# Kernel tuning notes

Hardware: AMD Instinct MI355X
Metric: run time of the kernel (lower is better)

The kernel has to match this reference:

```python
import jax, jax.numpy as jnp
import numpy as np

E, D, H, K = 8, 2048, 1024, 2  # num_experts, input_size, hidden_size, top_k
B, L = 2, 1024


def setup_inputs() -> dict:
    key = jax.random.key(0)
    k1, k2, k3, k4 = jax.random.split(key, 4)
    x = jax.random.normal(k1, (B, L, D), dtype=jnp.float32)
    w_gate = jax.random.normal(k2, (E, D), dtype=jnp.float32) * 0.02   # router Linear weight [E, D]
    w_in = jax.random.normal(k3, (E, 2 * H, D), dtype=jnp.float32) * 0.02  # ParallelExperts [E, out=2H, in=D]
    w_out = jax.random.normal(k4, (E, D, H), dtype=jnp.float32) * 0.02     # ParallelExperts [E, out=D, in=H]
    bias = jnp.zeros((D,), dtype=jnp.float32)
    return {"x": x, "w_gate": w_gate, "w_in": w_in, "w_out": w_out, "bias": bias}


def _moe_forward(x, w_gate, w_in, w_out, bias):
    bsz, length, d = x.shape
    xt = x.reshape(-1, d)  # [T, D]
    # top-k router: logits -> top-k -> softmax over selected logits
    logits = xt @ w_gate.T  # [T, E]
    topk_vals, topk_idx = jax.lax.top_k(logits, K)  # [T, K]
    topk_gates = jax.nn.softmax(topk_vals, axis=-1)  # [T, K]
    T = xt.shape[0]
    # dense [T, E] gate matrix; zero for non-selected experts, so the dense
    # per-expert compute below is mathematically identical to gathered dispatch
    gates = jnp.zeros((T, E), dtype=xt.dtype).at[jnp.arange(T)[:, None], topk_idx].add(topk_gates)
    # expert GLU FFN, vectorized over experts
    h = jnp.einsum('td,efd->tef', xt, w_in)  # [T, E, 2H]
    h1, h2 = jnp.split(h, 2, axis=-1)
    a = jax.nn.silu(h1) * h2                 # [T, E, H]
    eo = jnp.einsum('teh,edh->ted', a, w_out)  # [T, E, D]
    y = jnp.einsum('ted,te->td', eo, gates) + bias
    return y.reshape(bsz, length, d)


def reference(x, w_gate, w_in, w_out, bias):
    y = _moe_forward(x, w_gate, w_in, w_out, bias)
    loss = jnp.float32(0.0)  # router aux loss is 0 in eval mode (JetMoE top_k_gating)
    return (y, loss)
```

## Files before the change

kernel.cpp:

```cpp
#include <hip/hip_runtime.h>
#include <hip/hip_bf16.h>

#define E_    8
#define D_    2048
#define H_    1024
#define T_    2048
#define BK    64

using u16   = unsigned short;
using s16x8 = __attribute__((ext_vector_type(8))) short;
using f32x4 = __attribute__((ext_vector_type(4))) float;

#define WAITVM0 asm volatile("s_waitcnt vmcnt(0)" ::: "memory")

__device__ __forceinline__ short f2bf(float f) {
  __hip_bfloat16 h = __float2bfloat16(f);
  return __builtin_bit_cast(short, h);
}
__device__ __forceinline__ int slot(int r, int c) { return r * 64 + ((c ^ (r & 7)) << 3); }

__device__ __forceinline__ void gload16(const void* g, void* l) {
  __builtin_amdgcn_global_load_lds((const __attribute__((address_space(1))) void*)g,
                                   (__attribute__((address_space(3))) void*)l, 16, 0, 0);
}

#define FIND_EXPERT(ml, cnt, e, mt, Ne)                        \
  { int b_ = 0;                                                \
    _Pragma("unroll")                                          \
    for (int i_ = 0; i_ < E_; ++i_) {                          \
      int ti_ = (cnt[i_] + 127) >> 7;                          \
      if ((ml) >= b_ && (ml) < b_ + ti_) {                     \
        e = i_; mt = (ml) - b_; Ne = cnt[i_]; }                \
      b_ += ti_; } }


#define WIN_ELEMS  33554432
#define WTOT_ELEMS 50331648

__global__ __launch_bounds__(256) void prep_kernel(
    const float* __restrict__ x, const float* __restrict__ wg,
    const float* __restrict__ w_in, const float* __restrict__ w_out,
    const float* __restrict__ bias,
    u16* __restrict__ xb, u16* __restrict__ wb_in, u16* __restrict__ wb_out,
    int* __restrict__ lists, float* __restrict__ gates, int* __restrict__ counts,
    float* __restrict__ out)
{
  int t = blockIdx.x;
  int tid = threadIdx.x;

#pragma unroll
  for (int j = 0; j < 12; ++j) {
    int idx = t * 24576 + j * 2048 + tid * 8;
    const float* src; u16* dst;
    if (idx < WIN_ELEMS) { src = w_in + idx;  dst = wb_in + idx; }
    else                 { src = w_out + (idx - WIN_ELEMS); dst = wb_out + (idx - WIN_ELEMS); }
    f32x4 a = *(const f32x4*)(src);
    f32x4 b = *(const f32x4*)(src + 4);
    s16x8 o;
    o[0]=f2bf(a.x); o[1]=f2bf(a.y); o[2]=f2bf(a.z); o[3]=f2bf(a.w);
    o[4]=f2bf(b.x); o[5]=f2bf(b.y); o[6]=f2bf(b.z); o[7]=f2bf(b.w);
    *(s16x8*)dst = o;
  }

  {
    const float* bp = bias + tid * 8;
    f32x4 b0 = *(const f32x4*)(bp), b1 = *(const f32x4*)(bp + 4);
    *(f32x4*)(out + (size_t)t * D_ + tid * 8)     = b0;
    *(f32x4*)(out + (size_t)t * D_ + tid * 8 + 4) = b1;
    if (t == 0 && tid == 0) out[(size_t)T_ * D_] = 0.0f;
  }

  const float* xr = x + (size_t)t * D_;
  float acc[E_];
#pragma unroll
  for (int e = 0; e < E_; ++e) acc[e] = 0.f;
#pragma unroll
  for (int i = 0; i < D_ / 256; ++i) {
    int d = tid + 256 * i;
    float xv = xr[d];
    xb[(size_t)t * D_ + d] = (u16)f2bf(xv);
#pragma unroll
    for (int e = 0; e < E_; ++e) acc[e] += xv * wg[e * D_ + d];
  }
#pragma unroll
  for (int off = 32; off >= 1; off >>= 1)
#pragma unroll
    for (int e = 0; e < E_; ++e) acc[e] += __shfl_down(acc[e], off);

  __shared__ float red[4][E_];
  int w = tid >> 6, lane = tid & 63;
  if (lane == 0)
#pragma unroll
    for (int e = 0; e < E_; ++e) red[w][e] = acc[e];
  __syncthreads();
  if (tid == 0) {
    float v0 = -1e30f, v1 = -1e30f; int e0 = 0, e1 = 0;
#pragma unroll
    for (int e = 0; e < E_; ++e) {
      float v = red[0][e] + red[1][e] + red[2][e] + red[3][e];
      if (v > v0)      { v1 = v0; e1 = e0; v0 = v; e0 = e; }
      else if (v > v1) { v1 = v;  e1 = e; }
    }
    float g1 = expf(v1 - v0);
    float inv = 1.f / (1.f + g1);
    float g0 = inv; g1 *= inv;
    int s0 = atomicAdd(&counts[e0], 1);
    lists[e0 * T_ + s0] = t * 2 + 0;
    gates[t * 2 + 0] = g0;
    int s1 = atomicAdd(&counts[e1], 1);
    lists[e1 * T_ + s1] = t * 2 + 1;
    gates[t * 2 + 1] = g1;
  }
}

__global__ __launch_bounds__(512, 2) void gemm1_kernel(
    const u16* __restrict__ xb, const u16* __restrict__ wb_in,
    const int* __restrict__ lists, const int* __restrict__ counts,
    u16* __restrict__ a_buf)
{
  __shared__ __align__(16) u16 As[2][128 * 64];
  __shared__ __align__(16) u16 Bs[2][128 * 64];

  int cnt[E_];
#pragma unroll
  for (int i = 0; i < E_; ++i) cnt[i] = counts[i];
  int mt_total = 0;
#pragma unroll
  for (int i = 0; i < E_; ++i) mt_total += (cnt[i] + 127) >> 7;
  int total = mt_total * 16;
  int chunk = (total + 7) >> 3;

  int tid = threadIdx.x, w = tid >> 6, lane = tid & 63;
  int swzc = ((lane & 7) ^ (lane >> 3)) * 8;
  int wr = (w >> 2) * 64, wc = (w & 3) * 32, lrow = lane & 15, g = lane >> 4;
  int lcol = lane & 15, lr4 = (lane >> 4) * 4;
  int xcd = blockIdx.x & 7, bslot = blockIdx.x >> 3;

  for (int sl = bslot; sl < chunk; sl += 64) {
    int t = xcd * chunk + sl;
    if (t >= total) break;
    int ml = t >> 4, n = t & 15;
    int e = 0, mt = 0, Ne = 0;
    FIND_EXPERT(ml, cnt, e, mt, Ne);

    const u16* ap[2];
#pragma unroll
    for (int i = 0; i < 2; ++i) {
      int gr = mt * 128 + w * 8 + i * 64 + (lane >> 3);
      if (gr >= Ne) gr = Ne - 1;
      ap[i] = xb + (size_t)(lists[e * T_ + gr] >> 1) * D_ + swzc;
    }
    const u16* bp[2];
#pragma unroll
    for (int i = 0; i < 2; ++i) {
      int br = w * 8 + i * 64 + (lane >> 3);
      int o = n * 64 + ((br >> 4) & 1) * H_ + (br >> 5) * 16 + (br & 15);
      bp[i] = wb_in + (size_t)e * (2 * H_) * D_ + (size_t)o * D_ + swzc;
    }

    f32x4 acc[4][2];
#pragma unroll
    for (int m = 0; m < 4; ++m) { acc[m][0] = (f32x4){0,0,0,0}; acc[m][1] = (f32x4){0,0,0,0}; }

#pragma unroll
    for (int i = 0; i < 2; ++i) {
      gload16(ap[i], &As[0][(w * 8 + i * 64) * 64]);
      gload16(bp[i], &Bs[0][(w * 8 + i * 64) * 64]);
    }
    WAITVM0;
    __syncthreads();

    const int NT = D_ / BK;
    for (int kt = 0; kt < NT; ++kt) {
      int cur = kt & 1;
      if (kt + 1 < NT) {
        int k = (kt + 1) * BK;
#pragma unroll
        for (int i = 0; i < 2; ++i) {
          gload16(ap[i] + k, &As[cur ^ 1][(w * 8 + i * 64) * 64]);
          gload16(bp[i] + k, &Bs[cur ^ 1][(w * 8 + i * 64) * 64]);
        }
      }
#pragma unroll
      for (int ks = 0; ks < 2; ++ks) {
        int ch = ks * 4 + g;
        s16x8 af[4], bf[2];
#pragma unroll
        for (int m = 0; m < 4; ++m) af[m] = *(const s16x8*)(&As[cur][slot(wr + m * 16 + lrow, ch)]);
#pragma unroll
        for (int s = 0; s < 2; ++s)  bf[s] = *(const s16x8*)(&Bs[cur][slot(wc + s * 16 + lrow, ch)]);
#pragma unroll
        for (int m = 0; m < 4; ++m)
#pragma unroll
          for (int s = 0; s < 2; ++s)
            acc[m][s] = __builtin_amdgcn_mfma_f32_16x16x32_bf16(af[m], bf[s], acc[m][s], 0, 0, 0);
      }
      WAITVM0;
      __syncthreads();
    }
#pragma unroll
    for (int m = 0; m < 4; ++m)
#pragma unroll
      for (int q = 0; q < 4; ++q) {
        int row = mt * 128 + wr + m * 16 + lr4 + q;
        if (row < Ne) {
          float h1 = acc[m][0][q], h2 = acc[m][1][q];
          float a = (h1 / (1.f + __expf(-h1))) * h2;
          a_buf[((size_t)e * T_ + row) * H_ + n * 64 + (w & 3) * 16 + lcol] = (u16)f2bf(a);
        }
      }
  }
}

__global__ __launch_bounds__(512, 2) void gemm2_kernel(
    const u16* __restrict__ a_buf, const u16* __restrict__ wb_out,
    const int* __restrict__ lists, const int* __restrict__ counts,
    const float* __restrict__ gates, float* __restrict__ out)
{
  __shared__ __align__(16) u16 As[2][128 * 64];
  __shared__ __align__(16) u16 Bs[2][128 * 64];

  int cnt[E_];
#pragma unroll
  for (int i = 0; i < E_; ++i) cnt[i] = counts[i];
  int mt_total = 0;
#pragma unroll
  for (int i = 0; i < E_; ++i) mt_total += (cnt[i] + 127) >> 7;
  int total = mt_total * 16;
  int chunk = (total + 7) >> 3;

  int tid = threadIdx.x, w = tid >> 6, lane = tid & 63;
  int swzc = ((lane & 7) ^ (lane >> 3)) * 8;
  int wr = (w >> 2) * 64, wc = (w & 3) * 32, lrow = lane & 15, g = lane >> 4;
  int lcol = lane & 15, lr4 = (lane >> 4) * 4;
  int xcd = blockIdx.x & 7, bslot = blockIdx.x >> 3;

  for (int sl = bslot; sl < chunk; sl += 64) {
    int t = xcd * chunk + sl;
    if (t >= total) break;
    int ml = t >> 4, n = t & 15;
    int e = 0, mt = 0, Ne = 0;
    FIND_EXPERT(ml, cnt, e, mt, Ne);

    const u16* ap[2];
#pragma unroll
    for (int i = 0; i < 2; ++i) {
      int gr = mt * 128 + w * 8 + i * 64 + (lane >> 3);
      if (gr >= Ne) gr = Ne - 1;
      ap[i] = a_buf + ((size_t)e * T_ + gr) * H_ + swzc;
    }
    const u16* bp[2];
#pragma unroll
    for (int i = 0; i < 2; ++i) {
      int br = w * 8 + i * 64 + (lane >> 3);
      bp[i] = wb_out + (size_t)e * D_ * H_ + (size_t)(n * 128 + br) * H_ + swzc;
    }

    f32x4 acc[4][2];
#pragma unroll
    for (int m = 0; m < 4; ++m) { acc[m][0] = (f32x4){0,0,0,0}; acc[m][1] = (f32x4){0,0,0,0}; }

#pragma unroll
    for (int i = 0; i < 2; ++i) {
      gload16(ap[i], &As[0][(w * 8 + i * 64) * 64]);
      gload16(bp[i], &Bs[0][(w * 8 + i * 64) * 64]);
    }
    WAITVM0;
    __syncthreads();

    const int NT = H_ / BK;
    for (int kt = 0; kt < NT; ++kt) {
      int cur = kt & 1;
      if (kt + 1 < NT) {
        int k = (kt + 1) * BK;
#pragma unroll
        for (int i = 0; i < 2; ++i) {
          gload16(ap[i] + k, &As[cur ^ 1][(w * 8 + i * 64) * 64]);
          gload16(bp[i] + k, &Bs[cur ^ 1][(w * 8 + i * 64) * 64]);
        }
      }
#pragma unroll
      for (int ks = 0; ks < 2; ++ks) {
        int ch = ks * 4 + g;
        s16x8 af[4], bf[2];
#pragma unroll
        for (int m = 0; m < 4; ++m) af[m] = *(const s16x8*)(&As[cur][slot(wr + m * 16 + lrow, ch)]);
#pragma unroll
        for (int s = 0; s < 2; ++s)  bf[s] = *(const s16x8*)(&Bs[cur][slot(wc + s * 16 + lrow, ch)]);
#pragma unroll
        for (int m = 0; m < 4; ++m)
#pragma unroll
          for (int s = 0; s < 2; ++s)
            acc[m][s] = __builtin_amdgcn_mfma_f32_16x16x32_bf16(af[m], bf[s], acc[m][s], 0, 0, 0);
      }
      WAITVM0;
      __syncthreads();
    }
#pragma unroll
    for (int m = 0; m < 4; ++m)
#pragma unroll
      for (int q = 0; q < 4; ++q) {
        int row = mt * 128 + wr + m * 16 + lr4 + q;
        if (row < Ne) {
          int p = lists[e * T_ + row];
          float gt = gates[p];
          int tok = p >> 1;
#pragma unroll
          for (int s = 0; s < 2; ++s)
            atomicAdd(&out[(size_t)tok * D_ + n * 128 + wc + s * 16 + lcol], gt * acc[m][s][q]);
        }
      }
  }
}

extern "C" void kernel_launch(void* const* d_in, const int* in_sizes, int n_in,
                              void* d_out, int out_size, void* d_ws, size_t ws_size,
                              hipStream_t stream)
{
  const float* x      = (const float*)d_in[0];
  const float* w_gate = (const float*)d_in[1];
  const float* w_in   = (const float*)d_in[2];
  const float* w_out  = (const float*)d_in[3];
  const float* bias   = (const float*)d_in[4];
  float* out = (float*)d_out;

  char* ws = (char*)d_ws;
  u16*   xb     = (u16*)(ws);
  u16*   a_buf  = (u16*)(ws + 8388608);
  u16*   wb_in  = (u16*)(ws + 41943040);
  u16*   wb_out = (u16*)(ws + 109051904);
  int*   lists  = (int*)(ws + 142606336);
  float* gates  = (float*)(ws + 142671872);
  int*   counts = (int*)(ws + 142688256);

  hipMemsetAsync(counts, 0, E_ * sizeof(int), stream);
  prep_kernel<<<T_, 256, 0, stream>>>(x, w_gate, w_in, w_out, bias,
                                      xb, wb_in, wb_out, lists, gates, counts, out);
  gemm1_kernel<<<512, 512, 0, stream>>>(xb, wb_in, lists, counts, a_buf);
  gemm2_kernel<<<512, 512, 0, stream>>>(a_buf, wb_out, lists, counts, gates, out);
}
```

Before: 226.8 us.

## Use 256x64 GEMM tiles with paired M-tile scheduling and split weight conversion

Both expert GEMMs now use 256-row token tiles with 64-column weight tiles, so each weight tile is reused across more tokens and fewer weight bytes are streamed. Work items interleave two M-tiles per N index so neighbouring blocks share weight tiles in cache. Weight fp32-to-bf16 conversion moves out of the router kernel into separate grid-stride convert kernels. The cost is more padding waste for small experts, more LDS per block, and two extra kernel launches.

```diff
diff --git a/kernel.cpp b/kernel.cpp
--- a/kernel.cpp
+++ b/kernel.cpp
@@ -28,39 +28,42 @@
   { int b_ = 0;                                                \
     _Pragma("unroll")                                          \
     for (int i_ = 0; i_ < E_; ++i_) {                          \
-      int ti_ = (cnt[i_] + 127) >> 7;                          \
+      int ti_ = (cnt[i_] + 255) >> 8;                          \
       if ((ml) >= b_ && (ml) < b_ + ti_) {                     \
         e = i_; mt = (ml) - b_; Ne = cnt[i_]; }                \
       b_ += ti_; } }
 
 
 #define WIN_ELEMS  33554432
-#define WTOT_ELEMS 50331648
-
-__global__ __launch_bounds__(256) void prep_kernel(
+#define WOUT_ELEMS 16777216
+
+__global__ __launch_bounds__(256) void convert_kernel(
+    const float* __restrict__ src, u16* __restrict__ dst, int n)
+{
+  int stride = gridDim.x * 256 * 16;
+  for (int i = (blockIdx.x * 256 + threadIdx.x) * 16; i < n; i += stride) {
+    f32x4 a0 = *(const f32x4*)(src + i);
+    f32x4 a1 = *(const f32x4*)(src + i + 4);
+    f32x4 a2 = *(const f32x4*)(src + i + 8);
+    f32x4 a3 = *(const f32x4*)(src + i + 12);
+    s16x8 o0, o1;
+    o0[0]=f2bf(a0.x); o0[1]=f2bf(a0.y); o0[2]=f2bf(a0.z); o0[3]=f2bf(a0.w);
+    o0[4]=f2bf(a1.x); o0[5]=f2bf(a1.y); o0[6]=f2bf(a1.z); o0[7]=f2bf(a1.w);
+    o1[0]=f2bf(a2.x); o1[1]=f2bf(a2.y); o1[2]=f2bf(a2.z); o1[3]=f2bf(a2.w);
+    o1[4]=f2bf(a3.x); o1[5]=f2bf(a3.y); o1[6]=f2bf(a3.z); o1[7]=f2bf(a3.w);
+    *(s16x8*)(dst + i)     = o0;
+    *(s16x8*)(dst + i + 8) = o1;
+  }
+}
+
+__global__ __launch_bounds__(256) void router_kernel(
     const float* __restrict__ x, const float* __restrict__ wg,
-    const float* __restrict__ w_in, const float* __restrict__ w_out,
     const float* __restrict__ bias,
-    u16* __restrict__ xb, u16* __restrict__ wb_in, u16* __restrict__ wb_out,
-    int* __restrict__ lists, float* __restrict__ gates, int* __restrict__ counts,
-    float* __restrict__ out)
+    u16* __restrict__ xb, int* __restrict__ lists, float* __restrict__ gates,
+    int* __restrict__ counts, float* __restrict__ out)
 {
   int t = blockIdx.x;
   int tid = threadIdx.x;
-
-#pragma unroll
-  for (int j = 0; j < 12; ++j) {
-    int idx = t * 24576 + j * 2048 + tid * 8;
-    const float* src; u16* dst;
-    if (idx < WIN_ELEMS) { src = w_in + idx;  dst = wb_in + idx; }
-    else                 { src = w_out + (idx - WIN_ELEMS); dst = wb_out + (idx - WIN_ELEMS); }
-    f32x4 a = *(const f32x4*)(src);
-    f32x4 b = *(const f32x4*)(src + 4);
-    s16x8 o;
-    o[0]=f2bf(a.x); o[1]=f2bf(a.y); o[2]=f2bf(a.z); o[3]=f2bf(a.w);
-    o[4]=f2bf(b.x); o[5]=f2bf(b.y); o[6]=f2bf(b.z); o[7]=f2bf(b.w);
-    *(s16x8*)dst = o;
-  }
 
   {
     const float* bp = bias + tid * 8;
@@ -118,44 +121,46 @@
     const int* __restrict__ lists, const int* __restrict__ counts,
     u16* __restrict__ a_buf)
 {
-  __shared__ __align__(16) u16 As[2][128 * 64];
-  __shared__ __align__(16) u16 Bs[2][128 * 64];
+  __shared__ __align__(16) u16 As[2][256 * 64];
+  __shared__ __align__(16) u16 Bs[2][64 * 64];
 
   int cnt[E_];
 #pragma unroll
   for (int i = 0; i < E_; ++i) cnt[i] = counts[i];
   int mt_total = 0;
 #pragma unroll
-  for (int i = 0; i < E_; ++i) mt_total += (cnt[i] + 127) >> 7;
-  int total = mt_total * 16;
-  int chunk = (total + 7) >> 3;
+  for (int i = 0; i < E_; ++i) mt_total += (cnt[i] + 255) >> 8;
+  const int NN = 32;
+  int total_padded = ((mt_total + 1) >> 1) * (2 * NN);
+  int chunk = (total_padded + 7) >> 3;
 
   int tid = threadIdx.x, w = tid >> 6, lane = tid & 63;
   int swzc = ((lane & 7) ^ (lane >> 3)) * 8;
-  int wr = (w >> 2) * 64, wc = (w & 3) * 32, lrow = lane & 15, g = lane >> 4;
+  int wr = (w >> 1) * 64, wc = (w & 1) * 32, lrow = lane & 15, g = lane >> 4;
   int lcol = lane & 15, lr4 = (lane >> 4) * 4;
   int xcd = blockIdx.x & 7, bslot = blockIdx.x >> 3;
 
   for (int sl = bslot; sl < chunk; sl += 64) {
-    int t = xcd * chunk + sl;
-    if (t >= total) break;
-    int ml = t >> 4, n = t & 15;
+    int u = xcd * chunk + sl;
+    if (u >= total_padded) break;
+    int p = u / (2 * NN), q = u % (2 * NN);
+    int ml = p * 2 + (q & 1), n = q >> 1;
+    if (ml >= mt_total) continue;
     int e = 0, mt = 0, Ne = 0;
     FIND_EXPERT(ml, cnt, e, mt, Ne);
 
-    const u16* ap[2];
-#pragma unroll
-    for (int i = 0; i < 2; ++i) {
-      int gr = mt * 128 + w * 8 + i * 64 + (lane >> 3);
+    const u16* ap[4];
+#pragma unroll
+    for (int i = 0; i < 4; ++i) {
+      int gr = mt * 256 + w * 8 + i * 64 + (lane >> 3);
       if (gr >= Ne) gr = Ne - 1;
       ap[i] = xb + (size_t)(lists[e * T_ + gr] >> 1) * D_ + swzc;
     }
-    const u16* bp[2];
-#pragma unroll
-    for (int i = 0; i < 2; ++i) {
-      int br = w * 8 + i * 64 + (lane >> 3);
-      int o = n * 64 + ((br >> 4) & 1) * H_ + (br >> 5) * 16 + (br & 15);
-      bp[i] = wb_in + (size_t)e * (2 * H_) * D_ + (size_t)o * D_ + swzc;
+    const u16* bp;
+    {
+      int r = w * 8 + (lane >> 3);
+      int o = n * 32 + ((r >> 4) & 1) * H_ + (r >> 5) * 16 + (r & 15);
+      bp = wb_in + (size_t)e * (2 * H_) * D_ + (size_t)o * D_ + swzc;
     }
 
     f32x4 acc[4][2];
@@ -163,10 +168,8 @@
     for (int m = 0; m < 4; ++m) { acc[m][0] = (f32x4){0,0,0,0}; acc[m][1] = (f32x4){0,0,0,0}; }
 
 #pragma unroll
-    for (int i = 0; i < 2; ++i) {
-      gload16(ap[i], &As[0][(w * 8 + i * 64) * 64]);
-      gload16(bp[i], &Bs[0][(w * 8 + i * 64) * 64]);
-    }
+    for (int i = 0; i < 4; ++i) gload16(ap[i], &As[0][(w * 8 + i * 64) * 64]);
+    gload16(bp, &Bs[0][(w * 8) * 64]);
     WAITVM0;
     __syncthreads();
 
@@ -176,10 +179,8 @@
       if (kt + 1 < NT) {
         int k = (kt + 1) * BK;
 #pragma unroll
-        for (int i = 0; i < 2; ++i) {
-          gload16(ap[i] + k, &As[cur ^ 1][(w * 8 + i * 64) * 64]);
-          gload16(bp[i] + k, &Bs[cur ^ 1][(w * 8 + i * 64) * 64]);
-        }
+        for (int i = 0; i < 4; ++i) gload16(ap[i] + k, &As[cur ^ 1][(w * 8 + i * 64) * 64]);
+        gload16(bp + k, &Bs[cur ^ 1][(w * 8) * 64]);
       }
 #pragma unroll
       for (int ks = 0; ks < 2; ++ks) {
@@ -201,12 +202,13 @@
 #pragma unroll
     for (int m = 0; m < 4; ++m)
 #pragma unroll
-      for (int q = 0; q < 4; ++q) {
-        int row = mt * 128 + wr + m * 16 + lr4 + q;
+      for (int qq = 0; qq < 4; ++qq) {
+        int row = mt * 256 + wr + m * 16 + lr4 + qq;
         if (row < Ne) {
-          float h1 = acc[m][0][q], h2 = acc[m][1][q];
+          float h1 = acc[m][0][qq], h2 = acc[m][1][qq];
           float a = (h1 / (1.f + __expf(-h1))) * h2;
-          a_buf[((size_t)e * T_ + row) * H_ + n * 64 + (w & 3) * 16 + lcol] = (u16)f2bf(a);
+          int col = n * 32 + (w & 1) * 16 + lcol;
+          a_buf[((size_t)e * T_ + row) * H_ + col] = (u16)f2bf(a);
         }
       }
   }
@@ -217,43 +219,45 @@
     const int* __restrict__ lists, const int* __restrict__ counts,
     const float* __restrict__ gates, float* __restrict__ out)
 {
-  __shared__ __align__(16) u16 As[2][128 * 64];
-  __shared__ __align__(16) u16 Bs[2][128 * 64];
+  __shared__ __align__(16) u16 As[2][256 * 64];
+  __shared__ __align__(16) u16 Bs[2][64 * 64];
 
   int cnt[E_];
 #pragma unroll
   for (int i = 0; i < E_; ++i) cnt[i] = counts[i];
   int mt_total = 0;
 #pragma unroll
-  for (int i = 0; i < E_; ++i) mt_total += (cnt[i] + 127) >> 7;
-  int total = mt_total * 16;
-  int chunk = (total + 7) >> 3;
+  for (int i = 0; i < E_; ++i) mt_total += (cnt[i] + 255) >> 8;
+  const int NN = 32;
+  int total_padded = ((mt_total + 1) >> 1) * (2 * NN);
+  int chunk = (total_padded + 7) >> 3;
 
   int tid = threadIdx.x, w = tid >> 6, lane = tid & 63;
   int swzc = ((lane & 7) ^ (lane >> 3)) * 8;
-  int wr = (w >> 2) * 64, wc = (w & 3) * 32, lrow = lane & 15, g = lane >> 4;
+  int wr = (w >> 1) * 64, wc = (w & 1) * 32, lrow = lane & 15, g = lane >> 4;
   int lcol = lane & 15, lr4 = (lane >> 4) * 4;
   int xcd = blockIdx.x & 7, bslot = blockIdx.x >> 3;
 
   for (int sl = bslot; sl < chunk; sl += 64) {
-    int t = xcd * chunk + sl;
-    if (t >= total) break;
-    int ml = t >> 4, n = t & 15;
+    int u = xcd * chunk + sl;
+    if (u >= total_padded) break;
+    int p = u / (2 * NN), q = u % (2 * NN);
+    int ml = p * 2 + (q & 1), n = q >> 1;
+    if (ml >= mt_total) continue;
     int e = 0, mt = 0, Ne = 0;
     FIND_EXPERT(ml, cnt, e, mt, Ne);
 
-    const u16* ap[2];
-#pragma unroll
-    for (int i = 0; i < 2; ++i) {
-      int gr = mt * 128 + w * 8 + i * 64 + (lane >> 3);
+    const u16* ap[4];
+#pragma unroll
+    for (int i = 0; i < 4; ++i) {
+      int gr = mt * 256 + w * 8 + i * 64 + (lane >> 3);
       if (gr >= Ne) gr = Ne - 1;
       ap[i] = a_buf + ((size_t)e * T_ + gr) * H_ + swzc;
     }
-    const u16* bp[2];
-#pragma unroll
-    for (int i = 0; i < 2; ++i) {
-      int br = w * 8 + i * 64 + (lane >> 3);
-      bp[i] = wb_out + (size_t)e * D_ * H_ + (size_t)(n * 128 + br) * H_ + swzc;
+    const u16* bp;
+    {
+      int r = w * 8 + (lane >> 3);
+      bp = wb_out + (size_t)e * D_ * H_ + (size_t)(n * 64 + r) * H_ + swzc;
     }
 
     f32x4 acc[4][2];
@@ -261,10 +265,8 @@
     for (int m = 0; m < 4; ++m) { acc[m][0] = (f32x4){0,0,0,0}; acc[m][1] = (f32x4){0,0,0,0}; }
 
 #pragma unroll
-    for (int i = 0; i < 2; ++i) {
-      gload16(ap[i], &As[0][(w * 8 + i * 64) * 64]);
-      gload16(bp[i], &Bs[0][(w * 8 + i * 64) * 64]);
-    }
+    for (int i = 0; i < 4; ++i) gload16(ap[i], &As[0][(w * 8 + i * 64) * 64]);
+    gload16(bp, &Bs[0][(w * 8) * 64]);
     WAITVM0;
     __syncthreads();
 
@@ -274,10 +276,8 @@
       if (kt + 1 < NT) {
         int k = (kt + 1) * BK;
 #pragma unroll
-        for (int i = 0; i < 2; ++i) {
-          gload16(ap[i] + k, &As[cur ^ 1][(w * 8 + i * 64) * 64]);
-          gload16(bp[i] + k, &Bs[cur ^ 1][(w * 8 + i * 64) * 64]);
-        }
+        for (int i = 0; i < 4; ++i) gload16(ap[i] + k, &As[cur ^ 1][(w * 8 + i * 64) * 64]);
+        gload16(bp + k, &Bs[cur ^ 1][(w * 8) * 64]);
       }
 #pragma unroll
       for (int ks = 0; ks < 2; ++ks) {
@@ -299,15 +299,15 @@
 #pragma unroll
     for (int m = 0; m < 4; ++m)
 #pragma unroll
-      for (int q = 0; q < 4; ++q) {
-        int row = mt * 128 + wr + m * 16 + lr4 + q;
+      for (int qq = 0; qq < 4; ++qq) {
+        int row = mt * 256 + wr + m * 16 + lr4 + qq;
         if (row < Ne) {
-          int p = lists[e * T_ + row];
-          float gt = gates[p];
-          int tok = p >> 1;
+          int pp = lists[e * T_ + row];
+          float gt = gates[pp];
+          int tok = pp >> 1;
 #pragma unroll
           for (int s = 0; s < 2; ++s)
-            atomicAdd(&out[(size_t)tok * D_ + n * 128 + wc + s * 16 + lcol], gt * acc[m][s][q]);
+            atomicAdd(&out[(size_t)tok * D_ + n * 64 + wc + s * 16 + lcol], gt * acc[m][s][qq]);
         }
       }
   }
@@ -334,8 +334,9 @@
   int*   counts = (int*)(ws + 142688256);
 
   hipMemsetAsync(counts, 0, E_ * sizeof(int), stream);
-  prep_kernel<<<T_, 256, 0, stream>>>(x, w_gate, w_in, w_out, bias,
-                                      xb, wb_in, wb_out, lists, gates, counts, out);
+  convert_kernel<<<2048, 256, 0, stream>>>(w_in,  wb_in,  WIN_ELEMS);
+  convert_kernel<<<2048, 256, 0, stream>>>(w_out, wb_out, WOUT_ELEMS);
+  router_kernel<<<T_, 256, 0, stream>>>(x, w_gate, bias, xb, lists, gates, counts, out);
   gemm1_kernel<<<512, 512, 0, stream>>>(xb, wb_in, lists, counts, a_buf);
   gemm2_kernel<<<512, 512, 0, stream>>>(a_buf, wb_out, lists, counts, gates, out);
 }
```

Result: slower. 250.7 us (+10.5%).
